# Performance work log

Hardware: AMD Instinct MI355X
Metric: run time of the kernel (lower is better)

The kernel has to match this reference:

```python
import jax, jax.numpy as jnp
import numpy as np

EPS = 1e-12

def l2_normalize(x):
    # matches torch.nn.functional.normalize(p=2): x / max(||x||, eps)
    n = jnp.sqrt(jnp.sum(x * x, axis=-1, keepdims=True))
    return x / jnp.maximum(n, EPS)

def setup_inputs() -> dict:
    key = jax.random.key(0)
    k1, k2, k3, k4 = jax.random.split(key, 4)
    batch, n_neg, E, n_rel = 512, 2048, 256, 1000
    return {
        "head_emb": jax.random.normal(k1, (batch, E), dtype=jnp.float32),
        "tail_emb": jax.random.normal(k2, (1, n_neg, E), dtype=jnp.float32),
        "relation_embedding": jax.random.normal(k3, (n_rel, 2 * E), dtype=jnp.float32),
        "relation_id": jax.random.randint(k4, (batch,), 0, n_rel, dtype=jnp.int64),
    }

def reference(head_emb, tail_emb, relation_embedding, relation_id):
    # PairRE.score_tails with negative_sample_sharing=True, scoring_norm=2,
    # normalize_entities=True.
    E = head_emb.shape[-1]
    rel = relation_embedding[relation_id]          # (batch, 2E)
    r_h, r_t = rel[:, :E], rel[:, E:]              # (batch, E) each
    h = l2_normalize(head_emb)                     # (batch, E)
    t = l2_normalize(tail_emb)                     # (1, n_neg, E)
    t = t.reshape(1, -1, E)                        # negative sample sharing
    # diff: (batch, n_neg, E)
    diff = t * r_t[:, None, :] - (h * r_h)[:, None, :]
    # p=2 norm reduction over embedding dim -> (batch, n_neg)
    return -jnp.sqrt(jnp.sum(diff * diff, axis=-1))
```

## Files before the change

### kernel.cpp

```cpp
#include <hip/hip_runtime.h>
#include <hip/hip_bf16.h>


#define B_DIM 512
#define N_DIM 2048
#define E_DIM 256
#define K_DIM 512
#define NSTEP 16
#define FRAG_US 512

typedef __attribute__((ext_vector_type(8))) __bf16 bf16x8;
typedef __attribute__((ext_vector_type(4))) float f32x4;

__device__ inline ushort f2bf(float x) {
    __hip_bfloat16 h = __float2bfloat16(x);
    union { __hip_bfloat16 b; ushort u; } cv; cv.b = h; return cv.u;
}

__device__ inline float wave_sum(float v) {
#pragma unroll
    for (int m = 1; m < 64; m <<= 1) v += __shfl_xor(v, m, 64);
    return v;
}

__global__ __launch_bounds__(256) void prep_kernel(
        const float* __restrict__ head, const float* __restrict__ tail,
        const float* __restrict__ rel,  const int* __restrict__ rid,
        ushort* __restrict__ Tbig, ushort* __restrict__ Abig,
        float* __restrict__ cvec) {
    const int tid = threadIdx.x, lane = tid & 63, wv = tid >> 6;
    const int w = blockIdx.x * 4 + wv;
    const int s_ = lane >> 2, q = lane & 3;
    const int k0 = lane * 8;
    const bool sqr = (k0 < E_DIM);
    const int e0 = k0 & (E_DIM - 1);

    if (w < N_DIM) {
        const int n = w;
        const float* row = tail + (size_t)n * E_DIM;
        const float4 v4 = ((const float4*)row)[lane];
        const float s = wave_sum(v4.x * v4.x + v4.y * v4.y + v4.z * v4.z + v4.w * v4.w);
        const float inv = 1.0f / fmaxf(sqrtf(s), 1e-12f);
        const float4 f0 = *(const float4*)(row + e0);
        const float4 f1 = *(const float4*)(row + e0 + 4);
        const float v[8] = {f0.x, f0.y, f0.z, f0.w, f1.x, f1.y, f1.z, f1.w};
        ushort u[8];
#pragma unroll
        for (int j = 0; j < 8; ++j) {
            float x = v[j] * inv;
            if (sqr) x *= x;
            u[j] = f2bf(x);
        }
        const int g = n >> 4, m = n & 15;
        *(uint4*)(Tbig + (size_t)((g * 16 + s_) * 64 + q * 16 + m) * 8) = *(const uint4*)u;
    } else {
        const int b = w - N_DIM;
        const int id = rid[b];
        const float* hrow  = head + (size_t)b * E_DIM;
        const float* rhrow = rel + (size_t)id * (2 * E_DIM);
        const float* rtrow = rhrow + E_DIM;
        const float4 h4  = ((const float4*)hrow)[lane];
        const float4 rh4 = ((const float4*)rhrow)[lane];
        const float s1 = wave_sum(h4.x * h4.x + h4.y * h4.y + h4.z * h4.z + h4.w * h4.w);
        const float inv = 1.0f / fmaxf(sqrtf(s1), 1e-12f);
        const float p0 = h4.x * inv * rh4.x, p1 = h4.y * inv * rh4.y;
        const float p2 = h4.z * inv * rh4.z, p3 = h4.w * inv * rh4.w;
        const float s2 = wave_sum(p0 * p0 + p1 * p1 + p2 * p2 + p3 * p3);
        if (lane == 0) cvec[b] = s2;

        const float4 rt0 = *(const float4*)(rtrow + e0);
        const float4 rt1 = *(const float4*)(rtrow + e0 + 4);
        const float rt[8] = {rt0.x, rt0.y, rt0.z, rt0.w, rt1.x, rt1.y, rt1.z, rt1.w};
        float v[8];
        if (sqr) {
#pragma unroll
            for (int j = 0; j < 8; ++j) v[j] = rt[j] * rt[j];
        } else {
            const float4 h0 = *(const float4*)(hrow + e0);
            const float4 h1 = *(const float4*)(hrow + e0 + 4);
            const float4 r0 = *(const float4*)(rhrow + e0);
            const float4 r1 = *(const float4*)(rhrow + e0 + 4);
            const float hh[8] = {h0.x, h0.y, h0.z, h0.w, h1.x, h1.y, h1.z, h1.w};
            const float rr[8] = {r0.x, r0.y, r0.z, r0.w, r1.x, r1.y, r1.z, r1.w};
#pragma unroll
            for (int j = 0; j < 8; ++j) v[j] = -2.0f * rt[j] * (hh[j] * inv * rr[j]);
        }
        ushort u[8];
#pragma unroll
        for (int j = 0; j < 8; ++j) u[j] = f2bf(v[j]);
        const int g = b >> 4, m = b & 15;
        *(uint4*)(Abig + (size_t)((g * 16 + s_) * 64 + q * 16 + m) * 8) = *(const uint4*)u;
    }
}

__global__ __launch_bounds__(256) void score_kernel(
        const ushort* __restrict__ Tbig, const ushort* __restrict__ Abig,
        const float* __restrict__ cvec, float* __restrict__ out) {
    const int tid = threadIdx.x, lane = tid & 63, wv = tid >> 6;
    const int p_n = blockIdx.x, b_super = blockIdx.y;
    const int gA  = b_super * 2 + (wv & 1);
    const int gT0 = p_n * 4 + (wv >> 1) * 2;

    const ushort* Ab  = Abig + (size_t)gA * NSTEP * FRAG_US + lane * 8;
    const ushort* Tb0 = Tbig + (size_t)gT0 * NSTEP * FRAG_US + lane * 8;
    const ushort* Tb1 = Tb0 + (size_t)NSTEP * FRAG_US;

    f32x4 acc0 = {0.f, 0.f, 0.f, 0.f}, acc1 = {0.f, 0.f, 0.f, 0.f};

    bf16x8 a_c  = *(const bf16x8*)(Ab);
    bf16x8 b0_c = *(const bf16x8*)(Tb0);
    bf16x8 b1_c = *(const bf16x8*)(Tb1);
#pragma unroll
    for (int s = 0; s < NSTEP - 1; ++s) {
        const bf16x8 a_n  = *(const bf16x8*)(Ab  + (s + 1) * FRAG_US);
        const bf16x8 b0_n = *(const bf16x8*)(Tb0 + (s + 1) * FRAG_US);
        const bf16x8 b1_n = *(const bf16x8*)(Tb1 + (s + 1) * FRAG_US);
        acc0 = __builtin_amdgcn_mfma_f32_16x16x32_bf16(a_c, b0_c, acc0, 0, 0, 0);
        acc1 = __builtin_amdgcn_mfma_f32_16x16x32_bf16(a_c, b1_c, acc1, 0, 0, 0);
        a_c = a_n; b0_c = b0_n; b1_c = b1_n;
    }
    acc0 = __builtin_amdgcn_mfma_f32_16x16x32_bf16(a_c, b0_c, acc0, 0, 0, 0);
    acc1 = __builtin_amdgcn_mfma_f32_16x16x32_bf16(a_c, b1_c, acc1, 0, 0, 0);

    const int ml = lane & 15, q = lane >> 4;
    const int b0 = gA * 16;
    const int n0 = gT0 * 16;
#pragma unroll
    for (int r = 0; r < 4; ++r) {
        const int b = b0 + q * 4 + r;
        const float cb = cvec[b];
        out[(size_t)b * N_DIM + n0 + ml]      = -sqrtf(fmaxf(acc0[r] + cb, 0.f));
        out[(size_t)b * N_DIM + n0 + 16 + ml] = -sqrtf(fmaxf(acc1[r] + cb, 0.f));
    }
}

__device__ inline float block_reduce_sum_256(float v, float* buf) {
#pragma unroll
    for (int o = 32; o > 0; o >>= 1) v += __shfl_down(v, o, 64);
    const int lane = threadIdx.x & 63, wid = threadIdx.x >> 6;
    __syncthreads();
    if (lane == 0) buf[wid] = v;
    __syncthreads();
    return buf[0] + buf[1] + buf[2] + buf[3];
}

__global__ __launch_bounds__(256) void fallback_kernel(
        const float* __restrict__ head, const float* __restrict__ tail,
        const float* __restrict__ rel,  const int* __restrict__ rid,
        float* __restrict__ out) {
    __shared__ float Hh[E_DIM];
    __shared__ float RT[E_DIM];
    __shared__ float buf[4];
    const int b = blockIdx.x;
    const int tid = threadIdx.x;
    const float hv = head[(size_t)b * E_DIM + tid];
    const int id = rid[b];
    const float rh = rel[(size_t)id * (2 * E_DIM) + tid];
    const float rt = rel[(size_t)id * (2 * E_DIM) + E_DIM + tid];
    const float tot = block_reduce_sum_256(hv * hv, buf);
    const float inv = 1.0f / fmaxf(sqrtf(tot), 1e-12f);
    const float HhV = hv * inv * rh;
    Hh[tid] = HhV; RT[tid] = rt;
    const float c = block_reduce_sum_256(HhV * HhV, buf);
    __syncthreads();
    for (int n = tid; n < N_DIM; n += 256) {
        float S1 = 0.f, S2 = 0.f, Stt = 0.f;
        for (int e = 0; e < E_DIM; ++e) {
            const float tv = tail[(size_t)n * E_DIM + e];
            const float p = tv * RT[e];
            S1 += p * p; S2 += p * Hh[e]; Stt += tv * tv;
        }
        const float al = 1.0f / fmaxf(sqrtf(Stt), 1e-12f);
        const float x = al * al * S1 - 2.0f * al * S2 + c;
        out[(size_t)b * N_DIM + n] = -sqrtf(fmaxf(x, 0.f));
    }
}

extern "C" void kernel_launch(void* const* d_in, const int* in_sizes, int n_in,
                              void* d_out, int out_size, void* d_ws, size_t ws_size,
                              hipStream_t stream) {
    const float* head = (const float*)d_in[0];
    const float* tail = (const float*)d_in[1];
    const float* rel  = (const float*)d_in[2];
    const int*   rid  = (const int*)d_in[3];
    float* out = (float*)d_out;

    const size_t needT = (size_t)N_DIM * K_DIM * sizeof(ushort);
    const size_t needA = (size_t)B_DIM * K_DIM * sizeof(ushort);
    const size_t needC = (size_t)B_DIM * sizeof(float);
    if (ws_size >= needT + needA + needC) {
        ushort* Tbig = (ushort*)d_ws;
        ushort* Abig = Tbig + (size_t)N_DIM * K_DIM;
        float*  cvec = (float*)(Abig + (size_t)B_DIM * K_DIM);
        prep_kernel<<<(N_DIM + B_DIM) / 4, 256, 0, stream>>>(head, tail, rel, rid,
                                                             Tbig, Abig, cvec);
        dim3 grid(N_DIM / 64, B_DIM / 32);
        score_kernel<<<grid, 256, 0, stream>>>(Tbig, Abig, cvec, out);
    } else {
        fallback_kernel<<<B_DIM, 256, 0, stream>>>(head, tail, rel, rid, out);
    }
}
```

Measured before the change: 67.99 us.

## Fuse prep and MFMA scoring into one kernel with swizzled LDS fragments

Replaces the two-kernel prep plus score pipeline with a single fused kernel. Each 32x32 output tile block normalizes its own tail and head rows, packs the bf16 MFMA fragments into XOR-swizzled shared memory, then runs the MFMA reduction from LDS. This removes the global workspace round-trip and one kernel launch. In exchange it recomputes tail normalization for every batch tile (16x) and head prep for every tail tile (64x), which multiplies redundant global reads and ALU work. It also drops the workspace-size fallback path.

```diff
diff --git a/kernel.cpp b/kernel.cpp
--- a/kernel.cpp
+++ b/kernel.cpp
@@ -7,14 +7,13 @@
 #define E_DIM 256
 #define K_DIM 512
 #define NSTEP 16
-#define FRAG_US 512
 
 typedef __attribute__((ext_vector_type(8))) __bf16 bf16x8;
 typedef __attribute__((ext_vector_type(4))) float f32x4;
 
 __device__ inline ushort f2bf(float x) {
     __hip_bfloat16 h = __float2bfloat16(x);
-    union { __hip_bfloat16 b; ushort u; } cv; cv.b = h; return cv.u;
+    union { __hip_bfloat16 b; ushort u; } cv_; cv_.b = h; return cv_.u;
 }
 
 __device__ inline float wave_sum(float v) {
@@ -23,156 +22,116 @@
     return v;
 }
 
-__global__ __launch_bounds__(256) void prep_kernel(
+#define SWZ16(a) ((a) ^ (((a) >> 4) & 7))
+
+__global__ __launch_bounds__(256) void fused_kernel(
         const float* __restrict__ head, const float* __restrict__ tail,
         const float* __restrict__ rel,  const int* __restrict__ rid,
-        ushort* __restrict__ Tbig, ushort* __restrict__ Abig,
-        float* __restrict__ cvec) {
+        float* __restrict__ out) {
+    __shared__ ushort frag[4096 * 8];
+    __shared__ float cv[32];
+
     const int tid = threadIdx.x, lane = tid & 63, wv = tid >> 6;
-    const int w = blockIdx.x * 4 + wv;
+    const int bx = blockIdx.x, by = blockIdx.y;
     const int s_ = lane >> 2, q = lane & 3;
     const int k0 = lane * 8;
     const bool sqr = (k0 < E_DIM);
     const int e0 = k0 & (E_DIM - 1);
 
-    if (w < N_DIM) {
-        const int n = w;
-        const float* row = tail + (size_t)n * E_DIM;
-        const float4 v4 = ((const float4*)row)[lane];
-        const float s = wave_sum(v4.x * v4.x + v4.y * v4.y + v4.z * v4.z + v4.w * v4.w);
-        const float inv = 1.0f / fmaxf(sqrtf(s), 1e-12f);
-        const float4 f0 = *(const float4*)(row + e0);
-        const float4 f1 = *(const float4*)(row + e0 + 4);
-        const float v[8] = {f0.x, f0.y, f0.z, f0.w, f1.x, f1.y, f1.z, f1.w};
-        ushort u[8];
+    for (int i = 0; i < 16; ++i) {
+        const int r = wv + 4 * i;
+        if (r < 32) {
+            const int ln = r;
+            const int n = bx * 32 + ln;
+            const float* row = tail + (size_t)n * E_DIM;
+            const float4 v4 = ((const float4*)row)[lane];
+            const float ssum = wave_sum(v4.x * v4.x + v4.y * v4.y +
+                                        v4.z * v4.z + v4.w * v4.w);
+            const float inv = 1.0f / fmaxf(sqrtf(ssum), 1e-12f);
+            const float4 f0 = *(const float4*)(row + e0);
+            const float4 f1 = *(const float4*)(row + e0 + 4);
+            const float v[8] = {f0.x, f0.y, f0.z, f0.w, f1.x, f1.y, f1.z, f1.w};
+            ushort u[8];
 #pragma unroll
-        for (int j = 0; j < 8; ++j) {
-            float x = v[j] * inv;
-            if (sqr) x *= x;
-            u[j] = f2bf(x);
+            for (int j = 0; j < 8; ++j) {
+                float x = v[j] * inv;
+                if (sqr) x *= x;
+                u[j] = f2bf(x);
+            }
+            const int g = ln >> 4, m = ln & 15;
+            const int a16 = g * 1024 + s_ * 64 + q * 16 + m;
+            *(uint4*)(frag + (size_t)SWZ16(a16) * 8) = *(const uint4*)u;
+        } else {
+            const int lb = r - 32;
+            const int b = by * 32 + lb;
+            const int id = rid[b];
+            const float* hrow  = head + (size_t)b * E_DIM;
+            const float* rhrow = rel + (size_t)id * (2 * E_DIM);
+            const float* rtrow = rhrow + E_DIM;
+            const float4 h4  = ((const float4*)hrow)[lane];
+            const float4 rh4 = ((const float4*)rhrow)[lane];
+            const float s1 = wave_sum(h4.x * h4.x + h4.y * h4.y +
+                                      h4.z * h4.z + h4.w * h4.w);
+            const float inv = 1.0f / fmaxf(sqrtf(s1), 1e-12f);
+            const float p0 = h4.x * inv * rh4.x, p1 = h4.y * inv * rh4.y;
+            const float p2 = h4.z * inv * rh4.z, p3 = h4.w * inv * rh4.w;
+            const float s2 = wave_sum(p0 * p0 + p1 * p1 + p2 * p2 + p3 * p3);
+            if (lane == 0) cv[lb] = s2;
+
+            const float4 rt0 = *(const float4*)(rtrow + e0);
+            const float4 rt1 = *(const float4*)(rtrow + e0 + 4);
+            const float rt[8] = {rt0.x, rt0.y, rt0.z, rt0.w,
+                                 rt1.x, rt1.y, rt1.z, rt1.w};
+            float v[8];
+            if (sqr) {
+#pragma unroll
+                for (int j = 0; j < 8; ++j) v[j] = rt[j] * rt[j];
+            } else {
+                const float4 h0 = *(const float4*)(hrow + e0);
+                const float4 h1 = *(const float4*)(hrow + e0 + 4);
+                const float4 r0 = *(const float4*)(rhrow + e0);
+                const float4 r1 = *(const float4*)(rhrow + e0 + 4);
+                const float hh[8] = {h0.x, h0.y, h0.z, h0.w,
+                                     h1.x, h1.y, h1.z, h1.w};
+                const float rr[8] = {r0.x, r0.y, r0.z, r0.w,
+                                     r1.x, r1.y, r1.z, r1.w};
+#pragma unroll
+                for (int j = 0; j < 8; ++j)
+                    v[j] = -2.0f * rt[j] * (hh[j] * inv * rr[j]);
+            }
+            ushort u[8];
+#pragma unroll
+            for (int j = 0; j < 8; ++j) u[j] = f2bf(v[j]);
+            const int g = lb >> 4, m = lb & 15;
+            const int a16 = 2048 + g * 1024 + s_ * 64 + q * 16 + m;
+            *(uint4*)(frag + (size_t)SWZ16(a16) * 8) = *(const uint4*)u;
         }
-        const int g = n >> 4, m = n & 15;
-        *(uint4*)(Tbig + (size_t)((g * 16 + s_) * 64 + q * 16 + m) * 8) = *(const uint4*)u;
-    } else {
-        const int b = w - N_DIM;
-        const int id = rid[b];
-        const float* hrow  = head + (size_t)b * E_DIM;
-        const float* rhrow = rel + (size_t)id * (2 * E_DIM);
-        const float* rtrow = rhrow + E_DIM;
-        const float4 h4  = ((const float4*)hrow)[lane];
-        const float4 rh4 = ((const float4*)rhrow)[lane];
-        const float s1 = wave_sum(h4.x * h4.x + h4.y * h4.y + h4.z * h4.z + h4.w * h4.w);
-        const float inv = 1.0f / fmaxf(sqrtf(s1), 1e-12f);
-        const float p0 = h4.x * inv * rh4.x, p1 = h4.y * inv * rh4.y;
-        const float p2 = h4.z * inv * rh4.z, p3 = h4.w * inv * rh4.w;
-        const float s2 = wave_sum(p0 * p0 + p1 * p1 + p2 * p2 + p3 * p3);
-        if (lane == 0) cvec[b] = s2;
+    }
 
-        const float4 rt0 = *(const float4*)(rtrow + e0);
-        const float4 rt1 = *(const float4*)(rtrow + e0 + 4);
-        const float rt[8] = {rt0.x, rt0.y, rt0.z, rt0.w, rt1.x, rt1.y, rt1.z, rt1.w};
-        float v[8];
-        if (sqr) {
+    __syncthreads();
+
+    const int gAl = wv & 1;
+    const int gTl = wv >> 1;
+    const int baseA = 2048 + gAl * 1024;
+    const int baseT = gTl * 1024;
+
+    f32x4 acc = {0.f, 0.f, 0.f, 0.f};
 #pragma unroll
-            for (int j = 0; j < 8; ++j) v[j] = rt[j] * rt[j];
-        } else {
-            const float4 h0 = *(const float4*)(hrow + e0);
-            const float4 h1 = *(const float4*)(hrow + e0 + 4);
-            const float4 r0 = *(const float4*)(rhrow + e0);
-            const float4 r1 = *(const float4*)(rhrow + e0 + 4);
-            const float hh[8] = {h0.x, h0.y, h0.z, h0.w, h1.x, h1.y, h1.z, h1.w};
-            const float rr[8] = {r0.x, r0.y, r0.z, r0.w, r1.x, r1.y, r1.z, r1.w};
-#pragma unroll
-            for (int j = 0; j < 8; ++j) v[j] = -2.0f * rt[j] * (hh[j] * inv * rr[j]);
-        }
-        ushort u[8];
-#pragma unroll
-        for (int j = 0; j < 8; ++j) u[j] = f2bf(v[j]);
-        const int g = b >> 4, m = b & 15;
-        *(uint4*)(Abig + (size_t)((g * 16 + s_) * 64 + q * 16 + m) * 8) = *(const uint4*)u;
+    for (int s = 0; s < NSTEP; ++s) {
+        const int aA = baseA + s * 64 + lane;
+        const int aT = baseT + s * 64 + lane;
+        const bf16x8 fa = *(const bf16x8*)(frag + (size_t)SWZ16(aA) * 8);
+        const bf16x8 ft = *(const bf16x8*)(frag + (size_t)SWZ16(aT) * 8);
+        acc = __builtin_amdgcn_mfma_f32_16x16x32_bf16(fa, ft, acc, 0, 0, 0);
     }
-}
 
-__global__ __launch_bounds__(256) void score_kernel(
-        const ushort* __restrict__ Tbig, const ushort* __restrict__ Abig,
-        const float* __restrict__ cvec, float* __restrict__ out) {
-    const int tid = threadIdx.x, lane = tid & 63, wv = tid >> 6;
-    const int p_n = blockIdx.x, b_super = blockIdx.y;
-    const int gA  = b_super * 2 + (wv & 1);
-    const int gT0 = p_n * 4 + (wv >> 1) * 2;
-
-    const ushort* Ab  = Abig + (size_t)gA * NSTEP * FRAG_US + lane * 8;
-    const ushort* Tb0 = Tbig + (size_t)gT0 * NSTEP * FRAG_US + lane * 8;
-    const ushort* Tb1 = Tb0 + (size_t)NSTEP * FRAG_US;
-
-    f32x4 acc0 = {0.f, 0.f, 0.f, 0.f}, acc1 = {0.f, 0.f, 0.f, 0.f};
-
-    bf16x8 a_c  = *(const bf16x8*)(Ab);
-    bf16x8 b0_c = *(const bf16x8*)(Tb0);
-    bf16x8 b1_c = *(const bf16x8*)(Tb1);
-#pragma unroll
-    for (int s = 0; s < NSTEP - 1; ++s) {
-        const bf16x8 a_n  = *(const bf16x8*)(Ab  + (s + 1) * FRAG_US);
-        const bf16x8 b0_n = *(const bf16x8*)(Tb0 + (s + 1) * FRAG_US);
-        const bf16x8 b1_n = *(const bf16x8*)(Tb1 + (s + 1) * FRAG_US);
-        acc0 = __builtin_amdgcn_mfma_f32_16x16x32_bf16(a_c, b0_c, acc0, 0, 0, 0);
-        acc1 = __builtin_amdgcn_mfma_f32_16x16x32_bf16(a_c, b1_c, acc1, 0, 0, 0);
-        a_c = a_n; b0_c = b0_n; b1_c = b1_n;
-    }
-    acc0 = __builtin_amdgcn_mfma_f32_16x16x32_bf16(a_c, b0_c, acc0, 0, 0, 0);
-    acc1 = __builtin_amdgcn_mfma_f32_16x16x32_bf16(a_c, b1_c, acc1, 0, 0, 0);
-
-    const int ml = lane & 15, q = lane >> 4;
-    const int b0 = gA * 16;
-    const int n0 = gT0 * 16;
+    const int ml = lane & 15, qq = lane >> 4;
+    const int n = bx * 32 + gTl * 16 + ml;
 #pragma unroll
     for (int r = 0; r < 4; ++r) {
-        const int b = b0 + q * 4 + r;
-        const float cb = cvec[b];
-        out[(size_t)b * N_DIM + n0 + ml]      = -sqrtf(fmaxf(acc0[r] + cb, 0.f));
-        out[(size_t)b * N_DIM + n0 + 16 + ml] = -sqrtf(fmaxf(acc1[r] + cb, 0.f));
-    }
-}
-
-__device__ inline float block_reduce_sum_256(float v, float* buf) {
-#pragma unroll
-    for (int o = 32; o > 0; o >>= 1) v += __shfl_down(v, o, 64);
-    const int lane = threadIdx.x & 63, wid = threadIdx.x >> 6;
-    __syncthreads();
-    if (lane == 0) buf[wid] = v;
-    __syncthreads();
-    return buf[0] + buf[1] + buf[2] + buf[3];
-}
-
-__global__ __launch_bounds__(256) void fallback_kernel(
-        const float* __restrict__ head, const float* __restrict__ tail,
-        const float* __restrict__ rel,  const int* __restrict__ rid,
-        float* __restrict__ out) {
-    __shared__ float Hh[E_DIM];
-    __shared__ float RT[E_DIM];
-    __shared__ float buf[4];
-    const int b = blockIdx.x;
-    const int tid = threadIdx.x;
-    const float hv = head[(size_t)b * E_DIM + tid];
-    const int id = rid[b];
-    const float rh = rel[(size_t)id * (2 * E_DIM) + tid];
-    const float rt = rel[(size_t)id * (2 * E_DIM) + E_DIM + tid];
-    const float tot = block_reduce_sum_256(hv * hv, buf);
-    const float inv = 1.0f / fmaxf(sqrtf(tot), 1e-12f);
-    const float HhV = hv * inv * rh;
-    Hh[tid] = HhV; RT[tid] = rt;
-    const float c = block_reduce_sum_256(HhV * HhV, buf);
-    __syncthreads();
-    for (int n = tid; n < N_DIM; n += 256) {
-        float S1 = 0.f, S2 = 0.f, Stt = 0.f;
-        for (int e = 0; e < E_DIM; ++e) {
-            const float tv = tail[(size_t)n * E_DIM + e];
-            const float p = tv * RT[e];
-            S1 += p * p; S2 += p * Hh[e]; Stt += tv * tv;
-        }
-        const float al = 1.0f / fmaxf(sqrtf(Stt), 1e-12f);
-        const float x = al * al * S1 - 2.0f * al * S2 + c;
-        out[(size_t)b * N_DIM + n] = -sqrtf(fmaxf(x, 0.f));
+        const int bl = gAl * 16 + qq * 4 + r;
+        const float x = acc[r] + cv[bl];
+        out[(size_t)(by * 32 + bl) * N_DIM + n] = -sqrtf(fmaxf(x, 0.f));
     }
 }
 
@@ -184,19 +143,8 @@
     const float* rel  = (const float*)d_in[2];
     const int*   rid  = (const int*)d_in[3];
     float* out = (float*)d_out;
+    (void)d_ws; (void)ws_size;
 
-    const size_t needT = (size_t)N_DIM * K_DIM * sizeof(ushort);
-    const size_t needA = (size_t)B_DIM * K_DIM * sizeof(ushort);
-    const size_t needC = (size_t)B_DIM * sizeof(float);
-    if (ws_size >= needT + needA + needC) {
-        ushort* Tbig = (ushort*)d_ws;
-        ushort* Abig = Tbig + (size_t)N_DIM * K_DIM;
-        float*  cvec = (float*)(Abig + (size_t)B_DIM * K_DIM);
-        prep_kernel<<<(N_DIM + B_DIM) / 4, 256, 0, stream>>>(head, tail, rel, rid,
-                                                             Tbig, Abig, cvec);
-        dim3 grid(N_DIM / 64, B_DIM / 32);
-        score_kernel<<<grid, 256, 0, stream>>>(Tbig, Abig, cvec, out);
-    } else {
-        fallback_kernel<<<B_DIM, 256, 0, stream>>>(head, tail, rel, rid, out);
-    }
+    dim3 grid(N_DIM / 32, B_DIM / 32);
+    fused_kernel<<<grid, 256, 0, stream>>>(head, tail, rel, rid, out);
 }
```

Result: slower. 92.00 us (+35.3%).

## Fuse prep and score into one cooperative kernel with grid sync

Applied to the files above, without the earlier changes.

Merges the prep and scoring kernels into a single cooperative launch of 512 blocks. Each wave first prepares one T row (and one A row for the first 512 waves), then a grid-wide barrier is taken before the MFMA scoring tile runs. This removes one kernel launch and the gap between the two kernels. In exchange it pays for a grid-sync barrier and relies on cooperative launch succeeding, otherwise it falls back to the two-kernel path.

```diff
diff --git a/kernel.cpp b/kernel.cpp
--- a/kernel.cpp
+++ b/kernel.cpp
@@ -1,5 +1,6 @@
 #include <hip/hip_runtime.h>
 #include <hip/hip_bf16.h>
+#include <hip/hip_cooperative_groups.h>
 
 
 #define B_DIM 512
@@ -9,18 +10,146 @@
 #define NSTEP 16
 #define FRAG_US 512
 
+namespace cg = cooperative_groups;
+
 typedef __attribute__((ext_vector_type(8))) __bf16 bf16x8;
 typedef __attribute__((ext_vector_type(4))) float f32x4;
 
 __device__ inline ushort f2bf(float x) {
     __hip_bfloat16 h = __float2bfloat16(x);
-    union { __hip_bfloat16 b; ushort u; } cv; cv.b = h; return cv.u;
+    union { __hip_bfloat16 b; ushort u; } cv_; cv_.b = h; return cv_.u;
 }
 
 __device__ inline float wave_sum(float v) {
 #pragma unroll
     for (int m = 1; m < 64; m <<= 1) v += __shfl_xor(v, m, 64);
     return v;
+}
+
+__device__ __forceinline__ void prep_T_row(const float* __restrict__ tail,
+        ushort* __restrict__ Tbig, int n, int lane) {
+    const int s_ = lane >> 2, q = lane & 3;
+    const int k0 = lane * 8;
+    const bool sqr = (k0 < E_DIM);
+    const int e0 = k0 & (E_DIM - 1);
+    const float* row = tail + (size_t)n * E_DIM;
+    const float4 v4 = ((const float4*)row)[lane];
+    const float s = wave_sum(v4.x * v4.x + v4.y * v4.y + v4.z * v4.z + v4.w * v4.w);
+    const float inv = 1.0f / fmaxf(sqrtf(s), 1e-12f);
+    const float4 f0 = *(const float4*)(row + e0);
+    const float4 f1 = *(const float4*)(row + e0 + 4);
+    const float v[8] = {f0.x, f0.y, f0.z, f0.w, f1.x, f1.y, f1.z, f1.w};
+    ushort u[8];
+#pragma unroll
+    for (int j = 0; j < 8; ++j) {
+        float x = v[j] * inv;
+        if (sqr) x *= x;
+        u[j] = f2bf(x);
+    }
+    const int g = n >> 4, m = n & 15;
+    *(uint4*)(Tbig + (size_t)((g * 16 + s_) * 64 + q * 16 + m) * 8) = *(const uint4*)u;
+}
+
+__device__ __forceinline__ void prep_A_row(const float* __restrict__ head,
+        const float* __restrict__ rel, const int* __restrict__ rid,
+        ushort* __restrict__ Abig, float* __restrict__ cvec, int b, int lane) {
+    const int s_ = lane >> 2, q = lane & 3;
+    const int k0 = lane * 8;
+    const bool sqr = (k0 < E_DIM);
+    const int e0 = k0 & (E_DIM - 1);
+    const int id = rid[b];
+    const float* hrow  = head + (size_t)b * E_DIM;
+    const float* rhrow = rel + (size_t)id * (2 * E_DIM);
+    const float* rtrow = rhrow + E_DIM;
+    const float4 h4  = ((const float4*)hrow)[lane];
+    const float4 rh4 = ((const float4*)rhrow)[lane];
+    const float s1 = wave_sum(h4.x * h4.x + h4.y * h4.y + h4.z * h4.z + h4.w * h4.w);
+    const float inv = 1.0f / fmaxf(sqrtf(s1), 1e-12f);
+    const float p0 = h4.x * inv * rh4.x, p1 = h4.y * inv * rh4.y;
+    const float p2 = h4.z * inv * rh4.z, p3 = h4.w * inv * rh4.w;
+    const float s2 = wave_sum(p0 * p0 + p1 * p1 + p2 * p2 + p3 * p3);
+    if (lane == 0) cvec[b] = s2;
+
+    const float4 rt0 = *(const float4*)(rtrow + e0);
+    const float4 rt1 = *(const float4*)(rtrow + e0 + 4);
+    const float rt[8] = {rt0.x, rt0.y, rt0.z, rt0.w, rt1.x, rt1.y, rt1.z, rt1.w};
+    float v[8];
+    if (sqr) {
+#pragma unroll
+        for (int j = 0; j < 8; ++j) v[j] = rt[j] * rt[j];
+    } else {
+        const float4 h0 = *(const float4*)(hrow + e0);
+        const float4 h1 = *(const float4*)(hrow + e0 + 4);
+        const float4 r0 = *(const float4*)(rhrow + e0);
+        const float4 r1 = *(const float4*)(rhrow + e0 + 4);
+        const float hh[8] = {h0.x, h0.y, h0.z, h0.w, h1.x, h1.y, h1.z, h1.w};
+        const float rr[8] = {r0.x, r0.y, r0.z, r0.w, r1.x, r1.y, r1.z, r1.w};
+#pragma unroll
+        for (int j = 0; j < 8; ++j) v[j] = -2.0f * rt[j] * (hh[j] * inv * rr[j]);
+    }
+    ushort u[8];
+#pragma unroll
+    for (int j = 0; j < 8; ++j) u[j] = f2bf(v[j]);
+    const int g = b >> 4, m = b & 15;
+    *(uint4*)(Abig + (size_t)((g * 16 + s_) * 64 + q * 16 + m) * 8) = *(const uint4*)u;
+}
+
+__device__ __forceinline__ void score_tile(const ushort* __restrict__ Tbig,
+        const ushort* __restrict__ Abig, const float* __restrict__ cvec,
+        float* __restrict__ out, int p_n, int b_super, int wv, int lane) {
+    const int gA  = b_super * 2 + (wv & 1);
+    const int gT0 = p_n * 4 + (wv >> 1) * 2;
+
+    const ushort* Ab  = Abig + (size_t)gA * NSTEP * FRAG_US + lane * 8;
+    const ushort* Tb0 = Tbig + (size_t)gT0 * NSTEP * FRAG_US + lane * 8;
+    const ushort* Tb1 = Tb0 + (size_t)NSTEP * FRAG_US;
+
+    f32x4 acc0 = {0.f, 0.f, 0.f, 0.f}, acc1 = {0.f, 0.f, 0.f, 0.f};
+
+    bf16x8 a_c  = *(const bf16x8*)(Ab);
+    bf16x8 b0_c = *(const bf16x8*)(Tb0);
+    bf16x8 b1_c = *(const bf16x8*)(Tb1);
+#pragma unroll
+    for (int s = 0; s < NSTEP - 1; ++s) {
+        const bf16x8 a_n  = *(const bf16x8*)(Ab  + (s + 1) * FRAG_US);
+        const bf16x8 b0_n = *(const bf16x8*)(Tb0 + (s + 1) * FRAG_US);
+        const bf16x8 b1_n = *(const bf16x8*)(Tb1 + (s + 1) * FRAG_US);
+        acc0 = __builtin_amdgcn_mfma_f32_16x16x32_bf16(a_c, b0_c, acc0, 0, 0, 0);
+        acc1 = __builtin_amdgcn_mfma_f32_16x16x32_bf16(a_c, b1_c, acc1, 0, 0, 0);
+        a_c = a_n; b0_c = b0_n; b1_c = b1_n;
+    }
+    acc0 = __builtin_amdgcn_mfma_f32_16x16x32_bf16(a_c, b0_c, acc0, 0, 0, 0);
+    acc1 = __builtin_amdgcn_mfma_f32_16x16x32_bf16(a_c, b1_c, acc1, 0, 0, 0);
+
+    const int ml = lane & 15, qq = lane >> 4;
+    const int b0 = gA * 16;
+    const int n0 = gT0 * 16;
+#pragma unroll
+    for (int r = 0; r < 4; ++r) {
+        const int b = b0 + qq * 4 + r;
+        const float cb = cvec[b];
+        out[(size_t)b * N_DIM + n0 + ml]      = -sqrtf(fmaxf(acc0[r] + cb, 0.f));
+        out[(size_t)b * N_DIM + n0 + 16 + ml] = -sqrtf(fmaxf(acc1[r] + cb, 0.f));
+    }
+}
+
+__global__ __launch_bounds__(256) void coop_kernel(
+        const float* __restrict__ head, const float* __restrict__ tail,
+        const float* __restrict__ rel,  const int* __restrict__ rid,
+        ushort* __restrict__ Tbig, ushort* __restrict__ Abig,
+        float* __restrict__ cvec, float* __restrict__ out) {
+    const int tid = threadIdx.x, lane = tid & 63, wv = tid >> 6;
+    const int bx = blockIdx.x, by = blockIdx.y;
+    const int gw = ((by * 32 + bx) << 2) + wv;
+
+    prep_T_row(tail, Tbig, gw, lane);
+    if (gw < B_DIM) prep_A_row(head, rel, rid, Abig, cvec, gw, lane);
+
+    __threadfence();
+    cg::this_grid().sync();
+    __threadfence();
+
+    score_tile(Tbig, Abig, cvec, out, bx, by, wv, lane);
 }
 
 __global__ __launch_bounds__(256) void prep_kernel(
@@ -30,108 +159,15 @@
         float* __restrict__ cvec) {
     const int tid = threadIdx.x, lane = tid & 63, wv = tid >> 6;
     const int w = blockIdx.x * 4 + wv;
-    const int s_ = lane >> 2, q = lane & 3;
-    const int k0 = lane * 8;
-    const bool sqr = (k0 < E_DIM);
-    const int e0 = k0 & (E_DIM - 1);
-
-    if (w < N_DIM) {
-        const int n = w;
-        const float* row = tail + (size_t)n * E_DIM;
-        const float4 v4 = ((const float4*)row)[lane];
-        const float s = wave_sum(v4.x * v4.x + v4.y * v4.y + v4.z * v4.z + v4.w * v4.w);
-        const float inv = 1.0f / fmaxf(sqrtf(s), 1e-12f);
-        const float4 f0 = *(const float4*)(row + e0);
-        const float4 f1 = *(const float4*)(row + e0 + 4);
-        const float v[8] = {f0.x, f0.y, f0.z, f0.w, f1.x, f1.y, f1.z, f1.w};
-        ushort u[8];
-#pragma unroll
-        for (int j = 0; j < 8; ++j) {
-            float x = v[j] * inv;
-            if (sqr) x *= x;
-            u[j] = f2bf(x);
-        }
-        const int g = n >> 4, m = n & 15;
-        *(uint4*)(Tbig + (size_t)((g * 16 + s_) * 64 + q * 16 + m) * 8) = *(const uint4*)u;
-    } else {
-        const int b = w - N_DIM;
-        const int id = rid[b];
-        const float* hrow  = head + (size_t)b * E_DIM;
-        const float* rhrow = rel + (size_t)id * (2 * E_DIM);
-        const float* rtrow = rhrow + E_DIM;
-        const float4 h4  = ((const float4*)hrow)[lane];
-        const float4 rh4 = ((const float4*)rhrow)[lane];
-        const float s1 = wave_sum(h4.x * h4.x + h4.y * h4.y + h4.z * h4.z + h4.w * h4.w);
-        const float inv = 1.0f / fmaxf(sqrtf(s1), 1e-12f);
-        const float p0 = h4.x * inv * rh4.x, p1 = h4.y * inv * rh4.y;
-        const float p2 = h4.z * inv * rh4.z, p3 = h4.w * inv * rh4.w;
-        const float s2 = wave_sum(p0 * p0 + p1 * p1 + p2 * p2 + p3 * p3);
-        if (lane == 0) cvec[b] = s2;
-
-        const float4 rt0 = *(const float4*)(rtrow + e0);
-        const float4 rt1 = *(const float4*)(rtrow + e0 + 4);
-        const float rt[8] = {rt0.x, rt0.y, rt0.z, rt0.w, rt1.x, rt1.y, rt1.z, rt1.w};
-        float v[8];
-        if (sqr) {
-#pragma unroll
-            for (int j = 0; j < 8; ++j) v[j] = rt[j] * rt[j];
-        } else {
-            const float4 h0 = *(const float4*)(hrow + e0);
-            const float4 h1 = *(const float4*)(hrow + e0 + 4);
-            const float4 r0 = *(const float4*)(rhrow + e0);
-            const float4 r1 = *(const float4*)(rhrow + e0 + 4);
-            const float hh[8] = {h0.x, h0.y, h0.z, h0.w, h1.x, h1.y, h1.z, h1.w};
-            const float rr[8] = {r0.x, r0.y, r0.z, r0.w, r1.x, r1.y, r1.z, r1.w};
-#pragma unroll
-            for (int j = 0; j < 8; ++j) v[j] = -2.0f * rt[j] * (hh[j] * inv * rr[j]);
-        }
-        ushort u[8];
-#pragma unroll
-        for (int j = 0; j < 8; ++j) u[j] = f2bf(v[j]);
-        const int g = b >> 4, m = b & 15;
-        *(uint4*)(Abig + (size_t)((g * 16 + s_) * 64 + q * 16 + m) * 8) = *(const uint4*)u;
-    }
+    if (w < N_DIM) prep_T_row(tail, Tbig, w, lane);
+    else           prep_A_row(head, rel, rid, Abig, cvec, w - N_DIM, lane);
 }
 
 __global__ __launch_bounds__(256) void score_kernel(
         const ushort* __restrict__ Tbig, const ushort* __restrict__ Abig,
         const float* __restrict__ cvec, float* __restrict__ out) {
     const int tid = threadIdx.x, lane = tid & 63, wv = tid >> 6;
-    const int p_n = blockIdx.x, b_super = blockIdx.y;
-    const int gA  = b_super * 2 + (wv & 1);
-    const int gT0 = p_n * 4 + (wv >> 1) * 2;
-
-    const ushort* Ab  = Abig + (size_t)gA * NSTEP * FRAG_US + lane * 8;
-    const ushort* Tb0 = Tbig + (size_t)gT0 * NSTEP * FRAG_US + lane * 8;
-    const ushort* Tb1 = Tb0 + (size_t)NSTEP * FRAG_US;
-
-    f32x4 acc0 = {0.f, 0.f, 0.f, 0.f}, acc1 = {0.f, 0.f, 0.f, 0.f};
-
-    bf16x8 a_c  = *(const bf16x8*)(Ab);
-    bf16x8 b0_c = *(const bf16x8*)(Tb0);
-    bf16x8 b1_c = *(const bf16x8*)(Tb1);
-#pragma unroll
-    for (int s = 0; s < NSTEP - 1; ++s) {
-        const bf16x8 a_n  = *(const bf16x8*)(Ab  + (s + 1) * FRAG_US);
-        const bf16x8 b0_n = *(const bf16x8*)(Tb0 + (s + 1) * FRAG_US);
-        const bf16x8 b1_n = *(const bf16x8*)(Tb1 + (s + 1) * FRAG_US);
-        acc0 = __builtin_amdgcn_mfma_f32_16x16x32_bf16(a_c, b0_c, acc0, 0, 0, 0);
-        acc1 = __builtin_amdgcn_mfma_f32_16x16x32_bf16(a_c, b1_c, acc1, 0, 0, 0);
-        a_c = a_n; b0_c = b0_n; b1_c = b1_n;
-    }
-    acc0 = __builtin_amdgcn_mfma_f32_16x16x32_bf16(a_c, b0_c, acc0, 0, 0, 0);
-    acc1 = __builtin_amdgcn_mfma_f32_16x16x32_bf16(a_c, b1_c, acc1, 0, 0, 0);
-
-    const int ml = lane & 15, q = lane >> 4;
-    const int b0 = gA * 16;
-    const int n0 = gT0 * 16;
-#pragma unroll
-    for (int r = 0; r < 4; ++r) {
-        const int b = b0 + q * 4 + r;
-        const float cb = cvec[b];
-        out[(size_t)b * N_DIM + n0 + ml]      = -sqrtf(fmaxf(acc0[r] + cb, 0.f));
-        out[(size_t)b * N_DIM + n0 + 16 + ml] = -sqrtf(fmaxf(acc1[r] + cb, 0.f));
-    }
+    score_tile(Tbig, Abig, cvec, out, blockIdx.x, blockIdx.y, wv, lane);
 }
 
 __device__ inline float block_reduce_sum_256(float v, float* buf) {
@@ -192,10 +228,17 @@
         ushort* Tbig = (ushort*)d_ws;
         ushort* Abig = Tbig + (size_t)N_DIM * K_DIM;
         float*  cvec = (float*)(Abig + (size_t)B_DIM * K_DIM);
-        prep_kernel<<<(N_DIM + B_DIM) / 4, 256, 0, stream>>>(head, tail, rel, rid,
-                                                             Tbig, Abig, cvec);
         dim3 grid(N_DIM / 64, B_DIM / 32);
-        score_kernel<<<grid, 256, 0, stream>>>(Tbig, Abig, cvec, out);
+        void* args[] = {(void*)&head, (void*)&tail, (void*)&rel, (void*)&rid,
+                        (void*)&Tbig, (void*)&Abig, (void*)&cvec, (void*)&out};
+        hipError_t e = hipLaunchCooperativeKernel(
+                reinterpret_cast<const void*>(coop_kernel), grid, dim3(256),
+                args, 0, stream);
+        if (e != hipSuccess) {
+            prep_kernel<<<(N_DIM + B_DIM) / 4, 256, 0, stream>>>(
+                    head, tail, rel, rid, Tbig, Abig, cvec);
+            score_kernel<<<grid, 256, 0, stream>>>(Tbig, Abig, cvec, out);
+        }
     } else {
         fallback_kernel<<<B_DIM, 256, 0, stream>>>(head, tail, rel, rid, out);
     }
```

After: 219.8 us. +223.3%, slower.
